# Kernel tuning notes

Measured on AMD Instinct MI355X. Metric: run time of the kernel, lower is better.

The kernel has to match this reference:

```python
import jax, jax.numpy as jnp
import numpy as np

E = 256

def setup_inputs() -> dict:
    key = jax.random.key(0)
    ks = jax.random.split(key, 10)
    N, T_y, T_x = 8, 300, 160
    s = 1.0 / np.sqrt(E)  # torch-style uniform-ish init scale, keeps gates unsaturated
    return {
        "inputs": jax.random.normal(ks[0], (N, T_y, E // 2), jnp.float32),
        "memory": jax.random.normal(ks[1], (N, T_x, E), jnp.float32),
        "h0": jnp.zeros((1, N, E), jnp.float32),
        "Wih": jax.random.normal(ks[2], (3 * E, E // 2), jnp.float32) * s,
        "Whh": jax.random.normal(ks[3], (3 * E, E), jnp.float32) * s,
        "bih": jax.random.normal(ks[4], (3 * E,), jnp.float32) * s,
        "bhh": jax.random.normal(ks[5], (3 * E,), jnp.float32) * s,
        "W": jax.random.normal(ks[6], (E, E), jnp.float32) * s,
        "U": jax.random.normal(ks[7], (E, E), jnp.float32) * s,
        "v": jax.random.normal(ks[8], (E,), jnp.float32) * s,
    }


def reference(inputs, memory, h0, Wih, Whh, bih, bhh, W, U, v):
    # GRU (PyTorch gate order r, z, n), batch_first, single layer, unidirectional.
    def step(h, x_t):
        gi = x_t @ Wih.T + bih      # [N, 3E]
        gh = h @ Whh.T + bhh        # [N, 3E]
        ir, iz, i_n = jnp.split(gi, 3, axis=-1)
        hr, hz, hn = jnp.split(gh, 3, axis=-1)
        r = jax.nn.sigmoid(ir + hr)
        z = jax.nn.sigmoid(iz + hz)
        n = jnp.tanh(i_n + r * hn)
        h_new = (1.0 - z) * n + z * h
        return h_new, h_new

    h_last, outs = jax.lax.scan(step, h0[0], jnp.swapaxes(inputs, 0, 1))
    outputs = jnp.swapaxes(outs, 0, 1)   # [N, T_y, E]
    hidden = h_last[None]                # [1, N, E]

    # Bahdanau additive attention
    w = outputs @ W.T                    # [N, T_y, E]
    u = memory @ U.T                     # [N, T_x, E]
    # scores: v . tanh(w + u) broadcast over [N, T_y, T_x, E]
    scores = jnp.einsum('ntxe,e->ntx', jnp.tanh(w[:, :, None, :] + u[:, None, :, :]), v)
    attn_weights = jax.nn.softmax(scores, axis=2)  # [N, T_y, T_x]
    return attn_weights, outputs, hidden
```

## Files before the change

kernel.cpp:

```cpp
#include <hip/hip_runtime.h>


typedef _Float16 f16x2 __attribute__((ext_vector_type(2)));
typedef _Float16 f16x8 __attribute__((ext_vector_type(8)));
typedef float f32x4 __attribute__((ext_vector_type(4)));

__device__ __forceinline__ float fexp2(float x) { return __builtin_amdgcn_exp2f(x); }
__device__ __forceinline__ float frcp(float x) { return __builtin_amdgcn_rcpf(x); }
__device__ __forceinline__ float fsig(float x) {
    return frcp(1.0f + fexp2(x * -1.4426950408889634f));
}
__device__ __forceinline__ float ftanh(float x) {
    return 1.0f - 2.0f * frcp(1.0f + fexp2(x * 2.8853900817779268f));
}

__device__ __forceinline__ float pick4(f32x4 v, int s) {
    float ab = (s & 1) ? v[1] : v[0];
    float cd = (s & 1) ? v[3] : v[2];
    return (s & 2) ? cd : ab;
}

__global__ __launch_bounds__(256) void phase1_kernel(
    const float* __restrict__ Whh, unsigned* __restrict__ wd,
    const float* __restrict__ inputs, const float* __restrict__ Wih,
    float* __restrict__ gi, const float* __restrict__ bih,
    const float* __restrict__ bhh) {
    if (blockIdx.x < 384) {
        int gid = blockIdx.x * 256 + threadIdx.x;
        int i = gid >> 9, t = gid & 511;
        int fi = i >> 2, j = i & 3;
        int g = fi >> 4, m2 = (fi >> 3) & 1, ks = fi & 7;
        int w = t >> 6, l = t & 63;
        int row = 256 * g + 32 * w + 16 * m2 + (l & 15);
        int k = 32 * ks + 8 * (l >> 4) + 2 * j;
        union { unsigned u; f16x2 h; } cv;
        cv.h[0] = (_Float16)Whh[(size_t)row * 256 + k];
        cv.h[1] = (_Float16)Whh[(size_t)row * 256 + k + 1];
        wd[i * 512 + t] = cv.u;
        return;
    }
    int id = blockIdx.x - 384;
    const int n0 = (id % 12) * 64, m0 = (id / 12) * 64;
    __shared__ float Xs[32][65];
    __shared__ float Ws2[32][65];
    const int tid = threadIdx.x;
    const int tx = tid & 15, ty = tid >> 4;
    const int M = 2400, K = 128;
    float acc[4][4] = {};
    for (int k0 = 0; k0 < K; k0 += 32) {
#pragma unroll
        for (int i = 0; i < 8; ++i) {
            int e = tid + i * 256;
            int kk = e & 31, m = e >> 5;
            int row = m0 + m;
            Xs[kk][m] = (row < M) ? inputs[(size_t)row * K + k0 + kk] : 0.0f;
            Ws2[kk][m] = Wih[(size_t)(n0 + m) * K + k0 + kk];
        }
        __syncthreads();
#pragma unroll
        for (int kk = 0; kk < 32; ++kk) {
            float a[4], b[4];
#pragma unroll
            for (int i = 0; i < 4; ++i) a[i] = Xs[kk][ty * 4 + i];
#pragma unroll
            for (int j = 0; j < 4; ++j) b[j] = Ws2[kk][tx * 4 + j];
#pragma unroll
            for (int i = 0; i < 4; ++i)
#pragma unroll
                for (int j = 0; j < 4; ++j) acc[i][j] += a[i] * b[j];
        }
        __syncthreads();
    }
#pragma unroll
    for (int i = 0; i < 4; ++i) {
        int row = m0 + ty * 4 + i;
        if (row >= M) continue;
        int b = row / 300;
        int t = row - b * 300;
#pragma unroll
        for (int j = 0; j < 4; ++j) {
            int col = n0 + tx * 4 + j;
            float val = acc[i][j] + ((col < 512) ? (bih[col] + bhh[col]) : bih[col]);
            gi[(size_t)(t * 8 + b) * 768 + col] = val;
        }
    }
}

__global__ __launch_bounds__(256) void gemm_kernel(
    const float* __restrict__ X, const float* __restrict__ Wt,
    float* __restrict__ C, _Float16* __restrict__ C16,
    int M, int N, int K, int mode) {
    __shared__ float Xs[32][65];
    __shared__ float Ws2[32][65];
    const int n0 = blockIdx.x * 64, m0 = blockIdx.y * 64;
    const int tid = threadIdx.x;
    const int tx = tid & 15, ty = tid >> 4;
    float acc[4][4] = {};
    for (int k0 = 0; k0 < K; k0 += 32) {
#pragma unroll
        for (int i = 0; i < 8; ++i) {
            int e = tid + i * 256;
            int kk = e & 31, m = e >> 5;
            int row = m0 + m;
            Xs[kk][m] = (row < M) ? X[(size_t)row * K + k0 + kk] : 0.0f;
            Ws2[kk][m] = Wt[(size_t)(n0 + m) * K + k0 + kk];
        }
        __syncthreads();
#pragma unroll
        for (int kk = 0; kk < 32; ++kk) {
            float a[4], b[4];
#pragma unroll
            for (int i = 0; i < 4; ++i) a[i] = Xs[kk][ty * 4 + i];
#pragma unroll
            for (int j = 0; j < 4; ++j) b[j] = Ws2[kk][tx * 4 + j];
#pragma unroll
            for (int i = 0; i < 4; ++i)
#pragma unroll
                for (int j = 0; j < 4; ++j) acc[i][j] += a[i] * b[j];
        }
        __syncthreads();
    }
#pragma unroll
    for (int i = 0; i < 4; ++i) {
        int row = m0 + ty * 4 + i;
        if (row >= M) continue;
#pragma unroll
        for (int j = 0; j < 4; ++j) {
            int col = n0 + tx * 4 + j;
            if (mode == 2) C16[(size_t)row * N + col] = (_Float16)acc[i][j];
            else           C[(size_t)row * N + col] = acc[i][j];
        }
    }
}

__global__ __launch_bounds__(512, 1) void gru_fused(
    const float* __restrict__ gi, const unsigned* __restrict__ wd,
    const float* __restrict__ h0, const float* __restrict__ bhh,
    float* __restrict__ outs, float* __restrict__ hid,
    const float* __restrict__ memory, const float* __restrict__ Um,
    _Float16* __restrict__ u16, int do_u16) {
    if (blockIdx.x >= 8) {
        if (!do_u16) return;
        int id = blockIdx.x - 8;
        const int n0 = (id & 3) * 64, m0 = (id >> 2) * 64;
        __shared__ float Xs[32][65];
        __shared__ float Ws2[32][65];
        const int tid = threadIdx.x;
        const int tx = tid & 15, ty = (tid & 255) >> 4;
        float acc[4][4] = {};
        for (int k0 = 0; k0 < 256; k0 += 32) {
            if (tid < 256) {
#pragma unroll
                for (int i = 0; i < 8; ++i) {
                    int e = tid + i * 256;
                    int kk = e & 31, m = e >> 5;
                    Xs[kk][m] = memory[(size_t)(m0 + m) * 256 + k0 + kk];
                    Ws2[kk][m] = Um[(size_t)(n0 + m) * 256 + k0 + kk];
                }
            }
            __syncthreads();
            if (tid < 256) {
#pragma unroll
                for (int kk = 0; kk < 32; ++kk) {
                    float a[4], b[4];
#pragma unroll
                    for (int i = 0; i < 4; ++i) a[i] = Xs[kk][ty * 4 + i];
#pragma unroll
                    for (int j = 0; j < 4; ++j) b[j] = Ws2[kk][tx * 4 + j];
#pragma unroll
                    for (int i = 0; i < 4; ++i)
#pragma unroll
                        for (int j = 0; j < 4; ++j) acc[i][j] += a[i] * b[j];
                }
            }
            __syncthreads();
        }
        if (tid < 256) {
#pragma unroll
            for (int i = 0; i < 4; ++i)
#pragma unroll
                for (int j = 0; j < 4; ++j)
                    u16[(size_t)(m0 + ty * 4 + i) * 256 + n0 + tx * 4 + j] =
                        (_Float16)acc[i][j];
        }
        return;
    }
    const int b = blockIdx.x;
    const int t = threadIdx.x;
    const int w = t >> 6, l = t & 63;
    const int grp = l >> 4;
    const int sel = l & 7;
    const int hi = (l >> 3) & 1;
    const int m2s = sel >> 2, rsel = sel & 3;
    const int e = 32 * w + 16 * m2s + 4 * grp + rsel;

    __shared__ __align__(16) _Float16 hbuf[2][256];

    f16x8 wf[48];
#pragma unroll
    for (int fi = 0; fi < 48; ++fi) {
        union { unsigned u[4]; f16x8 v; } cv;
#pragma unroll
        for (int j = 0; j < 4; ++j) cv.u[j] = wd[(fi * 4 + j) * 512 + t];
        wf[fi] = cv.v;
    }

    float h = h0[b * 256 + e];
    float bn = bhh[512 + e];
    if (!hi) hbuf[0][e] = (_Float16)h;
    const float* gp = gi + b * 768;
    float* op = outs + (size_t)b * 76800 + e;

    float gr = gp[e], gz = gp[e + 256], gn = gp[e + 512];
    __syncthreads();

    for (int st = 0; st < 300; ++st) {
        int stn = (st < 299) ? st + 1 : st;
        const float* g = gp + (size_t)stn * 6144;
        float grn = g[e], gzn = g[e + 256], gnn = g[e + 512];

        const _Float16* hb = hbuf[st & 1];
        f16x8 hv0 = *(const f16x8*)(hb + 0 * 32 + 8 * grp);
        f16x8 hv1 = *(const f16x8*)(hb + 1 * 32 + 8 * grp);
        f16x8 hv2 = *(const f16x8*)(hb + 2 * 32 + 8 * grp);
        f16x8 hv3 = *(const f16x8*)(hb + 3 * 32 + 8 * grp);
        f16x8 hv4 = *(const f16x8*)(hb + 4 * 32 + 8 * grp);
        f16x8 hv5 = *(const f16x8*)(hb + 5 * 32 + 8 * grp);
        f16x8 hv6 = *(const f16x8*)(hb + 6 * 32 + 8 * grp);
        f16x8 hv7 = *(const f16x8*)(hb + 7 * 32 + 8 * grp);

        f32x4 aR0 = {0.f, 0.f, 0.f, 0.f}, aR1 = {0.f, 0.f, 0.f, 0.f};
        f32x4 aZ0 = {0.f, 0.f, 0.f, 0.f}, aZ1 = {0.f, 0.f, 0.f, 0.f};
        f32x4 aN0 = {0.f, 0.f, 0.f, 0.f}, aN1 = {0.f, 0.f, 0.f, 0.f};
#define KSTEP(ks, hv)                                                        \
        aR0 = __builtin_amdgcn_mfma_f32_16x16x32_f16(wf[0 * 8 + ks], hv, aR0, 0, 0, 0); \
        aR1 = __builtin_amdgcn_mfma_f32_16x16x32_f16(wf[1 * 8 + ks], hv, aR1, 0, 0, 0); \
        aZ0 = __builtin_amdgcn_mfma_f32_16x16x32_f16(wf[2 * 8 + ks], hv, aZ0, 0, 0, 0); \
        aZ1 = __builtin_amdgcn_mfma_f32_16x16x32_f16(wf[3 * 8 + ks], hv, aZ1, 0, 0, 0); \
        aN0 = __builtin_amdgcn_mfma_f32_16x16x32_f16(wf[4 * 8 + ks], hv, aN0, 0, 0, 0); \
        aN1 = __builtin_amdgcn_mfma_f32_16x16x32_f16(wf[5 * 8 + ks], hv, aN1, 0, 0, 0);
        KSTEP(0, hv0) KSTEP(1, hv1) KSTEP(2, hv2) KSTEP(3, hv3)
        KSTEP(4, hv4) KSTEP(5, hv5) KSTEP(6, hv6) KSTEP(7, hv7)
#undef KSTEP

        f32x4 vR = m2s ? aR1 : aR0;
        f32x4 vZ = m2s ? aZ1 : aZ0;
        f32x4 vN = m2s ? aN1 : aN0;
        float sr = pick4(vR, rsel);
        float sz = pick4(vZ, rsel);
        float sn = pick4(vN, rsel);

        float r = fsig(gr + sr);
        float z = fsig(gz + sz);
        float n = ftanh(gn + r * (sn + bn));
        h = n + z * (h - n);

        gr = grn; gz = gzn; gn = gnn;

        if (hi)
            op[st * 256] = h;
        else
            hbuf[(st + 1) & 1][e] = (_Float16)h;
        asm volatile("s_waitcnt lgkmcnt(0)\n\ts_barrier" ::: "memory");
    }
    if (!hi) hid[b * 256 + e] = h;
}

__global__ __launch_bounds__(256) void attn_kernel(
    const _Float16* __restrict__ u16, const float* __restrict__ wv,
    const float* __restrict__ v, float* __restrict__ attn) {
    const int tc = blockIdx.x, b = blockIdx.y;
    const int tid = threadIdx.x;
    __shared__ float wL[256], vL[256], sc[160], red[2];
    __shared__ unsigned uS[160 * 129];

    const unsigned* ug = (const unsigned*)(u16 + (size_t)b * 160 * 256);
    for (int i = tid; i < 20480; i += 256) {
        int row = i >> 7, wi = i & 127;
        uS[row * 129 + wi] = ug[i];
    }
    vL[tid] = v[tid];

    for (int ti = 0; ti < 10; ++ti) {
        int t = tc * 10 + ti;
        wL[tid] = wv[(size_t)(b * 300 + t) * 256 + tid];
        __syncthreads();
        float acc = 0.0f;
        if (tid < 160) {
            const unsigned* ur = uS + tid * 129;
#pragma unroll 8
            for (int e2 = 0; e2 < 128; ++e2) {
                union { unsigned uu; _Float16 hh[2]; } cv;
                cv.uu = ur[e2];
                int ee = e2 * 2;
                acc += vL[ee] * ftanh(wL[ee] + (float)cv.hh[0]);
                acc += vL[ee + 1] * ftanh(wL[ee + 1] + (float)cv.hh[1]);
            }
            sc[tid] = acc;
        }
        __syncthreads();
        if (tid < 64) {
            float m = -3.0e38f;
            for (int i = tid; i < 160; i += 64) m = fmaxf(m, sc[i]);
#pragma unroll
            for (int o = 32; o; o >>= 1) m = fmaxf(m, __shfl_xor(m, o));
            if (tid == 0) red[0] = m;
        }
        __syncthreads();
        float ee = 0.0f;
        if (tid < 160) {
            ee = fexp2((acc - red[0]) * 1.4426950408889634f);
            sc[tid] = ee;
        }
        __syncthreads();
        if (tid < 64) {
            float s = 0.0f;
            for (int i = tid; i < 160; i += 64) s += sc[i];
#pragma unroll
            for (int o = 32; o; o >>= 1) s += __shfl_xor(s, o);
            if (tid == 0) red[1] = s;
        }
        __syncthreads();
        if (tid < 160)
            attn[(size_t)(b * 300 + t) * 160 + tid] = ee * frcp(red[1]);
        __syncthreads();
    }
}

extern "C" void kernel_launch(void* const* d_in, const int* in_sizes, int n_in,
                              void* d_out, int out_size, void* d_ws, size_t ws_size,
                              hipStream_t stream) {
    const float* inputs = (const float*)d_in[0];
    const float* memory = (const float*)d_in[1];
    const float* h0 = (const float*)d_in[2];
    const float* Wih = (const float*)d_in[3];
    const float* Whh = (const float*)d_in[4];
    const float* bih = (const float*)d_in[5];
    const float* bhh = (const float*)d_in[6];
    const float* Wm = (const float*)d_in[7];
    const float* Um = (const float*)d_in[8];
    const float* vv = (const float*)d_in[9];

    float* out = (float*)d_out;
    float* out_attn = out;
    float* out_outputs = out + 384000;
    float* out_hidden = out + 998400;

    char* ws = (char*)d_ws;
    float* gi = (float*)ws;
    unsigned* wd = (unsigned*)(ws + 7372800);
    float* wbuf = (float*)(ws + 655360);

    const size_t U16_OFF = 7766016;
    const bool fuse_u16 = ws_size >= U16_OFF + 655360;
    _Float16* u16 = fuse_u16 ? (_Float16*)(ws + U16_OFF) : (_Float16*)ws;

    phase1_kernel<<<840, 256, 0, stream>>>(Whh, wd, inputs, Wih, gi, bih, bhh);
    gru_fused<<<fuse_u16 ? 88 : 8, 512, 0, stream>>>(
        gi, wd, h0, bhh, out_outputs, out_hidden, memory, Um, u16,
        fuse_u16 ? 1 : 0);
    if (!fuse_u16)
        gemm_kernel<<<dim3(4, 20), 256, 0, stream>>>(memory, Um, nullptr, u16,
                                                     1280, 256, 256, 2);
    gemm_kernel<<<dim3(4, 38), 256, 0, stream>>>(out_outputs, Wm, wbuf, nullptr,
                                                 2400, 256, 256, 0);
    attn_kernel<<<dim3(30, 8), 256, 0, stream>>>(u16, wbuf, vv, out_attn);
}
```

Before: 496.1 us.

## Overlap attention with GRU recurrence via flag-synchronized persistent blocks

Fuses the W projection GEMM and the attention/softmax computation into the GRU kernel's spare blocks. These blocks spin on per-batch progress flags published every 32 steps, so attention for earlier timesteps runs while the sequential recurrence is still going. This removes two kernel launches and the serial tail after the GRU. In exchange it relies on all 88 blocks being co-resident and adds atomics, spin-waits and a larger shared-memory footprint per block, which could interfere with the latency-critical GRU blocks.

```diff
diff --git a/kernel.cpp b/kernel.cpp
--- a/kernel.cpp
+++ b/kernel.cpp
@@ -24,7 +24,8 @@
     const float* __restrict__ Whh, unsigned* __restrict__ wd,
     const float* __restrict__ inputs, const float* __restrict__ Wih,
     float* __restrict__ gi, const float* __restrict__ bih,
-    const float* __restrict__ bhh) {
+    const float* __restrict__ bhh, int* flags, int full) {
+    if (full && blockIdx.x == 0 && threadIdx.x < 10) flags[threadIdx.x] = 0;
     if (blockIdx.x < 384) {
         int gid = blockIdx.x * 256 + threadIdx.x;
         int i = gid >> 9, t = gid & 511;
@@ -133,19 +134,27 @@
     }
 }
 
-__global__ __launch_bounds__(512, 1) void gru_fused(
+__global__ __launch_bounds__(512, 1) void gru_mega(
     const float* __restrict__ gi, const unsigned* __restrict__ wd,
     const float* __restrict__ h0, const float* __restrict__ bhh,
     float* __restrict__ outs, float* __restrict__ hid,
     const float* __restrict__ memory, const float* __restrict__ Um,
-    _Float16* __restrict__ u16, int do_u16) {
+    _Float16* __restrict__ u16, const float* __restrict__ W,
+    const float* __restrict__ vv, float* __restrict__ attn,
+    int* flags, int full) {
+    __shared__ __align__(16) _Float16 hbuf[2][256];
+    __shared__ float Xs[32][65];
+    __shared__ float Ws2[32][65];
+    __shared__ unsigned uS[160 * 129];
+    __shared__ __align__(16) float oL[10][260];
+    __shared__ float wLf[10][256];
+    __shared__ float vL[256], sc[160], red[2];
+
+    const int tid = threadIdx.x;
+
     if (blockIdx.x >= 8) {
-        if (!do_u16) return;
         int id = blockIdx.x - 8;
         const int n0 = (id & 3) * 64, m0 = (id >> 2) * 64;
-        __shared__ float Xs[32][65];
-        __shared__ float Ws2[32][65];
-        const int tid = threadIdx.x;
         const int tx = tid & 15, ty = (tid & 255) >> 4;
         float acc[4][4] = {};
         for (int k0 = 0; k0 < 256; k0 += 32) {
@@ -183,10 +192,110 @@
                     u16[(size_t)(m0 + ty * 4 + i) * 256 + n0 + tx * 4 + j] =
                         (_Float16)acc[i][j];
         }
+        if (!full) return;
+        __syncthreads();
+        if (tid == 0)
+            __hip_atomic_fetch_add(&flags[8], 1, __ATOMIC_RELEASE,
+                                   __HIP_MEMORY_SCOPE_AGENT);
+
+        const int grp = id / 10;
+        const int jj = id % 10;
+        if (tid == 0) {
+            while (__hip_atomic_load(&flags[8], __ATOMIC_ACQUIRE,
+                                     __HIP_MEMORY_SCOPE_AGENT) < 80)
+                __builtin_amdgcn_s_sleep(64);
+        }
+        __syncthreads();
+        const unsigned* ug = (const unsigned*)(u16 + (size_t)grp * 160 * 256);
+        for (int i = tid; i < 20480; i += 512)
+            uS[(i >> 7) * 129 + (i & 127)] = ug[i];
+        if (tid < 256) vL[tid] = vv[tid];
+        __syncthreads();
+
+        for (int uu = 0; uu < 3; ++uu) {
+            const int tc = jj + uu * 10;
+            const int need = tc * 10 + 10;
+            if (tid == 0) {
+                while (__hip_atomic_load(&flags[grp], __ATOMIC_ACQUIRE,
+                                         __HIP_MEMORY_SCOPE_AGENT) < need)
+                    __builtin_amdgcn_s_sleep(64);
+            }
+            __syncthreads();
+            for (int i = tid; i < 2560; i += 512) {
+                int ti = i >> 8, k = i & 255;
+                oL[ti][k] = outs[((size_t)grp * 300 + tc * 10 + ti) * 256 + k];
+            }
+            __syncthreads();
+            if (tid < 256) {
+                float a0 = 0, a1 = 0, a2 = 0, a3 = 0, a4 = 0;
+                float a5 = 0, a6 = 0, a7 = 0, a8 = 0, a9 = 0;
+                for (int k4 = 0; k4 < 256; k4 += 4) {
+                    float4 wq = *(const float4*)(W + (size_t)tid * 256 + k4);
+#define WROW(ACC, TI)                                                     \
+                    {                                                     \
+                        float4 oq = *(const float4*)(&oL[TI][k4]);        \
+                        ACC += wq.x * oq.x + wq.y * oq.y +                \
+                               wq.z * oq.z + wq.w * oq.w;                 \
+                    }
+                    WROW(a0, 0) WROW(a1, 1) WROW(a2, 2) WROW(a3, 3) WROW(a4, 4)
+                    WROW(a5, 5) WROW(a6, 6) WROW(a7, 7) WROW(a8, 8) WROW(a9, 9)
+#undef WROW
+                }
+                wLf[0][tid] = a0; wLf[1][tid] = a1; wLf[2][tid] = a2;
+                wLf[3][tid] = a3; wLf[4][tid] = a4; wLf[5][tid] = a5;
+                wLf[6][tid] = a6; wLf[7][tid] = a7; wLf[8][tid] = a8;
+                wLf[9][tid] = a9;
+            }
+            __syncthreads();
+            for (int ti = 0; ti < 10; ++ti) {
+                int t = tc * 10 + ti;
+                float acc2 = 0.0f;
+                if (tid < 160) {
+                    const unsigned* ur = uS + tid * 129;
+                    const float* wl = wLf[ti];
+#pragma unroll 8
+                    for (int e2 = 0; e2 < 128; ++e2) {
+                        union { unsigned uu2; _Float16 hh[2]; } cv;
+                        cv.uu2 = ur[e2];
+                        int ee = e2 * 2;
+                        acc2 += vL[ee] * ftanh(wl[ee] + (float)cv.hh[0]);
+                        acc2 += vL[ee + 1] * ftanh(wl[ee + 1] + (float)cv.hh[1]);
+                    }
+                    sc[tid] = acc2;
+                }
+                __syncthreads();
+                if (tid < 64) {
+                    float m = -3.0e38f;
+                    for (int i = tid; i < 160; i += 64) m = fmaxf(m, sc[i]);
+#pragma unroll
+                    for (int o = 32; o; o >>= 1) m = fmaxf(m, __shfl_xor(m, o));
+                    if (tid == 0) red[0] = m;
+                }
+                __syncthreads();
+                float ee = 0.0f;
+                if (tid < 160) {
+                    ee = fexp2((acc2 - red[0]) * 1.4426950408889634f);
+                    sc[tid] = ee;
+                }
+                __syncthreads();
+                if (tid < 64) {
+                    float s = 0.0f;
+                    for (int i = tid; i < 160; i += 64) s += sc[i];
+#pragma unroll
+                    for (int o = 32; o; o >>= 1) s += __shfl_xor(s, o);
+                    if (tid == 0) red[1] = s;
+                }
+                __syncthreads();
+                if (tid < 160)
+                    attn[(size_t)(grp * 300 + t) * 160 + tid] = ee * frcp(red[1]);
+                __syncthreads();
+            }
+        }
         return;
     }
+
     const int b = blockIdx.x;
-    const int t = threadIdx.x;
+    const int t = tid;
     const int w = t >> 6, l = t & 63;
     const int grp = l >> 4;
     const int sel = l & 7;
@@ -194,8 +303,6 @@
     const int m2s = sel >> 2, rsel = sel & 3;
     const int e = 32 * w + 16 * m2s + 4 * grp + rsel;
 
-    __shared__ __align__(16) _Float16 hbuf[2][256];
-
     f16x8 wf[48];
 #pragma unroll
     for (int fi = 0; fi < 48; ++fi) {
@@ -215,6 +322,13 @@
     __syncthreads();
 
     for (int st = 0; st < 300; ++st) {
+        if (full && (st & 31) == 0 && st) {
+            asm volatile("s_waitcnt vmcnt(0)" ::: "memory");
+            __syncthreads();
+            if (t == 0)
+                __hip_atomic_store(&flags[b], st, __ATOMIC_RELEASE,
+                                   __HIP_MEMORY_SCOPE_AGENT);
+        }
         int stn = (st < 299) ? st + 1 : st;
         const float* g = gp + (size_t)stn * 6144;
         float grn = g[e], gzn = g[e + 256], gnn = g[e + 512];
@@ -263,6 +377,13 @@
             hbuf[(st + 1) & 1][e] = (_Float16)h;
         asm volatile("s_waitcnt lgkmcnt(0)\n\ts_barrier" ::: "memory");
     }
+    if (full) {
+        asm volatile("s_waitcnt vmcnt(0)" ::: "memory");
+        __syncthreads();
+        if (t == 0)
+            __hip_atomic_store(&flags[b], 300, __ATOMIC_RELEASE,
+                               __HIP_MEMORY_SCOPE_AGENT);
+    }
     if (!hi) hid[b * 256 + e] = h;
 }
 
@@ -275,10 +396,8 @@
     __shared__ unsigned uS[160 * 129];
 
     const unsigned* ug = (const unsigned*)(u16 + (size_t)b * 160 * 256);
-    for (int i = tid; i < 20480; i += 256) {
-        int row = i >> 7, wi = i & 127;
-        uS[row * 129 + wi] = ug[i];
-    }
+    for (int i = tid; i < 20480; i += 256)
+        uS[(i >> 7) * 129 + (i & 127)] = ug[i];
     vL[tid] = v[tid];
 
     for (int ti = 0; ti < 10; ++ti) {
@@ -349,20 +468,27 @@
     char* ws = (char*)d_ws;
     float* gi = (float*)ws;
     unsigned* wd = (unsigned*)(ws + 7372800);
-    float* wbuf = (float*)(ws + 655360);
-
-    const size_t U16_OFF = 7766016;
-    const bool fuse_u16 = ws_size >= U16_OFF + 655360;
-    _Float16* u16 = fuse_u16 ? (_Float16*)(ws + U16_OFF) : (_Float16*)ws;
-
-    phase1_kernel<<<840, 256, 0, stream>>>(Whh, wd, inputs, Wih, gi, bih, bhh);
-    gru_fused<<<fuse_u16 ? 88 : 8, 512, 0, stream>>>(
-        gi, wd, h0, bhh, out_outputs, out_hidden, memory, Um, u16,
-        fuse_u16 ? 1 : 0);
-    if (!fuse_u16)
+
+    const size_t U16_OFF = 7766016, FLAG_OFF = 8421376;
+    const bool full = ws_size >= FLAG_OFF + 64;
+    _Float16* u16 = full ? (_Float16*)(ws + U16_OFF) : (_Float16*)ws;
+    int* flags = (int*)(ws + FLAG_OFF);
+
+    phase1_kernel<<<840, 256, 0, stream>>>(Whh, wd, inputs, Wih, gi, bih, bhh,
+                                           flags, full ? 1 : 0);
+    if (full) {
+        gru_mega<<<88, 512, 0, stream>>>(gi, wd, h0, bhh, out_outputs,
+                                         out_hidden, memory, Um, u16, Wm, vv,
+                                         out_attn, flags, 1);
+    } else {
+        float* wbuf = (float*)(ws + 655360);
+        gru_mega<<<8, 512, 0, stream>>>(gi, wd, h0, bhh, out_outputs,
+                                        out_hidden, memory, Um, u16, Wm, vv,
+                                        out_attn, flags, 0);
         gemm_kernel<<<dim3(4, 20), 256, 0, stream>>>(memory, Um, nullptr, u16,
                                                      1280, 256, 256, 2);
-    gemm_kernel<<<dim3(4, 38), 256, 0, stream>>>(out_outputs, Wm, wbuf, nullptr,
-                                                 2400, 256, 256, 0);
-    attn_kernel<<<dim3(30, 8), 256, 0, stream>>>(u16, wbuf, vv, out_attn);
-}
+        gemm_kernel<<<dim3(4, 38), 256, 0, stream>>>(out_outputs, Wm, wbuf,
+                                                     nullptr, 2400, 256, 256, 0);
+        attn_kernel<<<dim3(30, 8), 256, 0, stream>>>(u16, wbuf, vv, out_attn);
+    }
+}
```

After: 489.5 us. No clear change (-1.3%).
